# Kernel optimization log

Measured on AMD Instinct MI355X. Metric: run time of the kernel, lower is better.

## Reference

```python
import jax, jax.numpy as jnp
import numpy as np

EPS = 1e-08


def setup_inputs() -> dict:
    key = jax.random.key(0)
    k1, k2 = jax.random.split(key)
    query_features = jax.random.normal(k1, (64, 1024, 32, 32), dtype=jnp.float32)
    support_features = jax.random.normal(k2, (25, 1024, 32, 32), dtype=jnp.float32)
    return {"query_features": query_features, "support_features": support_features}


def reference(query_features, support_features):
    B, C, h, w = support_features.shape
    NQ = query_features.shape[0]
    # Covariance over channels: flatten support to (C, B*h*w), center, GEMM.
    support = jnp.transpose(support_features, (1, 0, 2, 3)).reshape(C, -1)
    centered = support - jnp.mean(support, axis=1, keepdims=True)
    N = B * h * w
    cov = (centered @ centered.T) / (N - 1 + EPS)  # (C, C)
    # Queries: (NQ, C, d), L2-normalize each channel row over spatial dim.
    q = query_features.reshape(NQ, C, -1)
    q = q / (jnp.linalg.norm(q, axis=2, keepdims=True) + EPS)
    # diag(q^T cov q) without materializing (d, d): cov@q then elementwise reduce over C.
    cq = jnp.einsum('cD,nDd->ncd', cov, q)  # (NQ, C, d)
    scores = jnp.mean(jnp.sum(q * cq, axis=1), axis=1)  # (NQ,)
    return scores
```

## Files before the change

### kernel.cpp

```cpp
#include <hip/hip_runtime.h>

#define NQ   64
#define CCH  1024
#define DSP  1024
#define NSUP 25600
#define NK_COV 50

typedef __attribute__((ext_vector_type(4))) float f32x4;
typedef __attribute__((ext_vector_type(8))) __bf16 bf16x8;

#define WAITVM(N) asm volatile("s_waitcnt vmcnt(" #N ")" ::: "memory")
#define WAITLGKM0() asm volatile("s_waitcnt lgkmcnt(0)" ::: "memory")
#define BAR() __builtin_amdgcn_s_barrier()
#define SCHED0() __builtin_amdgcn_sched_barrier(0)

__device__ inline unsigned short f2bf(float x) {
  unsigned u = __builtin_bit_cast(unsigned, x);
  u += 0x7fffu + ((u >> 16) & 1u);
  return (unsigned short)(u >> 16);
}

__global__ __launch_bounds__(256) void zero_kernel(float4* __restrict__ cov4,
                                                   float4* __restrict__ out4) {
  const int i = blockIdx.x * 256 + threadIdx.x;
  cov4[i] = make_float4(0.f, 0.f, 0.f, 0.f);
  if (i < 16) out4[i] = make_float4(0.f, 0.f, 0.f, 0.f);
}


__global__ __launch_bounds__(512) void mean_center_kernel(
    const float* __restrict__ sup, float* __restrict__ mean,
    unsigned short* __restrict__ Sb, int write_sb) {
  __shared__ float4 row[6400];
  __shared__ float red[512];
  const int c = blockIdx.x;
  const int tid = threadIdx.x;
  float s = 0.f;
  for (int qd = tid; qd < 6400; qd += 512) {
    const int b = qd >> 8, s4 = (qd & 255) << 2;
    const float4 v = *(const float4*)(sup + ((size_t)b * CCH + c) * DSP + s4);
    row[qd] = v;
    s += v.x + v.y + v.z + v.w;
  }
  red[tid] = s;
  __syncthreads();
  for (int st = 256; st > 0; st >>= 1) {
    if (tid < st) red[tid] += red[tid + st];
    __syncthreads();
  }
  const float m = red[0] * (1.0f / 25600.0f);
  if (tid == 0) mean[c] = m;
  if (write_sb) {
    for (int qd = tid; qd < 6400; qd += 512) {
      const float4 v = row[qd];
      const int b = qd >> 8, s4 = (qd & 255) << 2;
      ushort4 o;
      o.x = f2bf(v.x - m); o.y = f2bf(v.y - m);
      o.z = f2bf(v.z - m); o.w = f2bf(v.w - m);
      *(ushort4*)(Sb + (size_t)c * NSUP + b * DSP + s4) = o;
    }
  }
}

__global__ __launch_bounds__(256) void qnorm_kernel(
    const float* __restrict__ q, float* __restrict__ qfac,
    unsigned short* __restrict__ Qb, int write_qb) {
  const int row = blockIdx.x * 4 + (threadIdx.x >> 6);
  const int l = threadIdx.x & 63;
  const float4* src = (const float4*)(q + (size_t)row * DSP);
  float4 v[4];
  float ss = 0.f;
#pragma unroll
  for (int i = 0; i < 4; ++i) {
    v[i] = src[l + 64 * i];
    ss += v[i].x * v[i].x + v[i].y * v[i].y + v[i].z * v[i].z + v[i].w * v[i].w;
  }
#pragma unroll
  for (int off = 32; off > 0; off >>= 1) ss += __shfl_xor(ss, off);
  const float f = 1.0f / (sqrtf(ss) + 1e-8f);
  if (l == 0) qfac[row] = f;
  if (write_qb) {
#pragma unroll
    for (int i = 0; i < 4; ++i) {
      ushort4 o;
      o.x = f2bf(v[i].x * f); o.y = f2bf(v[i].y * f);
      o.z = f2bf(v[i].z * f); o.w = f2bf(v[i].w * f);
      *(ushort4*)(Qb + (size_t)row * DSP + (size_t)(l + 64 * i) * 4) = o;
    }
  }
}


__device__ inline void rd4(const unsigned short* base, int r0, int col, int lr, bf16x8 f[4]) {
#pragma unroll
  for (int i = 0; i < 4; ++i)
    f[i] = *(const bf16x8*)(const void*)(base + (r0 + i * 16 + lr) * 64 + col);
}
__device__ inline void mfma16(const bf16x8 a[4], const bf16x8 b[4], f32x4 (*acc)[4]) {
  __builtin_amdgcn_s_setprio(1);
#pragma unroll
  for (int i = 0; i < 4; ++i)
#pragma unroll
    for (int j = 0; j < 4; ++j)
      acc[i][j] = __builtin_amdgcn_mfma_f32_16x16x32_bf16(a[i], b[j], acc[i][j], 0, 0, 0);
  __builtin_amdgcn_s_setprio(0);
}

__device__ inline void stage_glds(const unsigned short* __restrict__ src, int ld,
                                  int row0, int k0, unsigned short* lds) {
  const int tid = threadIdx.x;
  const int w = tid >> 6;
#pragma unroll
  for (int it = 0; it < 4; ++it) {
    const int ci = it * 256 + tid;
    const int r = ci >> 3;
    const int kc = ((ci & 7) ^ (r & 7)) << 3;
    const unsigned short* g = src + (size_t)(row0 + r) * ld + k0 + kc;
    unsigned short* lb = lds + ((it * 256 + w * 64) << 3);
    __builtin_amdgcn_global_load_lds((const __attribute__((address_space(1))) void*)g,
                                     (__attribute__((address_space(3))) void*)lb,
                                     16, 0, 0);
  }
}

__device__ inline void stage256g(const unsigned short* __restrict__ src, int ld,
                                 int row0, int k0, unsigned short* lds_base) {
  const int tid = threadIdx.x;
  const int wid = tid >> 6;
#pragma unroll
  for (int it = 0; it < 4; ++it) {
    const int ci = it * 512 + tid;
    const int r = ci >> 3;
    const int kc = ((ci & 7) ^ (r & 7)) << 3;
    const unsigned short* g = src + (size_t)(row0 + r) * ld + k0 + kc;
    unsigned short* lb = lds_base + ((it * 512 + (wid << 6)) << 3);
    __builtin_amdgcn_global_load_lds((const __attribute__((address_space(1))) void*)g,
                                     (__attribute__((address_space(3))) void*)lb,
                                     16, 0, 0);
  }
}

template <int NT>
__device__ inline void loop256(const unsigned short* __restrict__ src, int ld,
                               int rowA, int rowB, int k0, bool diag,
                               unsigned short* lds,
                               int wm, int wn, int lr, int kg, int sw,
                               f32x4 (*acc)[4]) {
  stage256g(src, ld, rowA, k0, lds);
  if (!diag) stage256g(src, ld, rowB, k0, lds + 16384);
  stage256g(src, ld, rowA, k0 + 64, lds + 32768);
  if (!diag) stage256g(src, ld, rowB, k0 + 64, lds + 32768 + 16384);

  for (int t = 0; t < NT; ++t) {
    const int cb = (t & 1) << 15;
    if (t < NT - 1) { if (diag) { WAITVM(4); } else { WAITVM(8); } }
    else { WAITVM(0); }
    BAR(); SCHED0();
    const unsigned short* A = lds + cb + wm * 8192;
    const unsigned short* B = lds + cb + (diag ? 0 : 16384) + (wn >> 1) * 8192;
    const int brow = (wn & 1) * 64;
    bf16x8 a[4], b[4];
    {
      const int col = kg ^ sw;
      rd4(B, brow, col, lr, b);
      rd4(A, 0, col, lr, a);
      mfma16(a, b, &acc[0]);
      rd4(A, 64, col, lr, a);
      mfma16(a, b, &acc[4]);
    }
    {
      const int col = (32 + kg) ^ sw;
      rd4(B, brow, col, lr, b);
      rd4(A, 0, col, lr, a);
      mfma16(a, b, &acc[0]);
      rd4(A, 64, col, lr, a);
      WAITLGKM0();
      BAR(); SCHED0();
      if (t + 2 < NT) {
        stage256g(src, ld, rowA, k0 + (t + 2) * 64, lds + cb);
        if (!diag) stage256g(src, ld, rowB, k0 + (t + 2) * 64, lds + cb + 16384);
      }
      mfma16(a, b, &acc[4]);
    }
  }
}

__device__ inline void decode_tile8(int t, int& ti, int& tj) {
  int rem = t; ti = 0;
  while (rem >= 8 - ti) { rem -= 8 - ti; ++ti; }
  tj = ti + rem;
}
__device__ inline void decode_pair4(int p, int& ti, int& tj) {
  int rem = p; ti = 0;
  while (rem >= 4 - ti) { rem -= 4 - ti; ++ti; }
  tj = ti + rem;
}

__global__ __launch_bounds__(256) void cov128_kernel(
    const unsigned short* __restrict__ Sb, float* __restrict__ cov) {
  __shared__ unsigned short clds[32768];
  const int wg = blockIdx.x;
  const int ks = wg & 7;
  int ti, tj; decode_tile8(wg >> 3, ti, tj);
  const bool diag = (ti == tj);
  const bool mirror = (!(ti & 1)) && (tj == ti + 1);
  const int tid = threadIdx.x, l = tid & 63, w = tid >> 6;
  const int wr = (w >> 1) * 64, wc = (w & 1) * 64, lr = l & 15, kg = (l >> 4) * 8;
  const int sw = (lr & 7) << 3;
  f32x4 acc[4][4];
#pragma unroll
  for (int i = 0; i < 4; ++i)
#pragma unroll
    for (int j = 0; j < 4; ++j) acc[i][j] = 0.f;

  const int kbase = ks * (NSUP / 8);

  stage_glds(Sb, NSUP, ti * 128, kbase, clds);
  if (!diag) stage_glds(Sb, NSUP, tj * 128, kbase, clds + 8192);
  stage_glds(Sb, NSUP, ti * 128, kbase + 64, clds + 16384);
  if (!diag) stage_glds(Sb, NSUP, tj * 128, kbase + 64, clds + 16384 + 8192);
  for (int t = 0; t < NK_COV; ++t) {
    const int cb = (t & 1) * 16384;
    if (t < NK_COV - 1) { if (diag) { WAITVM(4); } else { WAITVM(8); } }
    else { WAITVM(0); }
    BAR(); SCHED0();
    const unsigned short* A = clds + cb;
    const unsigned short* B = diag ? A : A + 8192;
    bf16x8 a[4], b[4];
    {
      const int col = kg ^ sw;
      rd4(A, wr, col, lr, a);
      rd4(B, wc, col, lr, b);
      mfma16(a, b, (f32x4(*)[4])acc);
    }
    {
      const int col = (32 + kg) ^ sw;
      rd4(A, wr, col, lr, a);
      rd4(B, wc, col, lr, b);
      WAITLGKM0();
      BAR(); SCHED0();
      if (t + 2 < NK_COV) {
        const int k2 = kbase + (t + 2) * 64;
        stage_glds(Sb, NSUP, ti * 128, k2, clds + cb);
        if (!diag) stage_glds(Sb, NSUP, tj * 128, k2, clds + cb + 8192);
      }
      mfma16(a, b, (f32x4(*)[4])acc);
    }
  }

  const float scale = 1.0f / (25599.0f + 1e-8f);
  const int rbase = ti * 128 + wr + (l >> 4) * 4;
  const int cbase = tj * 128 + wc + (l & 15);
#pragma unroll
  for (int i = 0; i < 4; ++i)
#pragma unroll
    for (int j = 0; j < 4; ++j)
#pragma unroll
      for (int r = 0; r < 4; ++r) {
        const float v = acc[i][j][r] * scale;
        atomicAdd(&cov[(size_t)(rbase + i * 16 + r) * CCH + cbase + j * 16], v);
        if (mirror)
          atomicAdd(&cov[(size_t)(cbase + j * 16) * CCH + rbase + i * 16 + r], v);
      }
}

__global__ __launch_bounds__(512, 2) void gram256_kernel(
    const unsigned short* __restrict__ Qb, const float* __restrict__ cov,
    float* __restrict__ out) {
  __shared__ unsigned short lds[65536];
  const int wg = blockIdx.x;
  const int xcd = wg & 7, slot = wg >> 3;
  const int n = xcd * 8 + slot / 10;
  int ti, tj; decode_pair4(slot % 10, ti, tj);
  const bool diag = (ti == tj);
  const int tid = threadIdx.x, l = tid & 63, wid = tid >> 6;
  const int wm = wid >> 2, wn = wid & 3;
  const int lr = l & 15, kg = (l >> 4) * 8;
  const int sw = (lr & 7) << 3;
  const unsigned short* Qn = Qb + (size_t)n * CCH * DSP;

  f32x4 acc[8][4];
#pragma unroll
  for (int i = 0; i < 8; ++i)
#pragma unroll
    for (int j = 0; j < 4; ++j) acc[i][j] = 0.f;

  loop256<16>(Qn, DSP, ti * 256, tj * 256, 0, diag, lds,
              wm, wn, lr, kg, sw, acc);

  float s = 0.f;
  const int rbase = ti * 256 + wm * 128 + (l >> 4) * 4;
  const int cbase = tj * 256 + wn * 64 + (l & 15);
#pragma unroll
  for (int i = 0; i < 8; ++i)
#pragma unroll
    for (int j = 0; j < 4; ++j)
#pragma unroll
      for (int r = 0; r < 4; ++r)
        s += acc[i][j][r] * cov[(size_t)(rbase + i * 16 + r) * CCH + cbase + j * 16];
  if (!diag) s *= 2.0f;
  s *= (1.0f / 1024.0f);
#pragma unroll
  for (int off = 32; off > 0; off >>= 1) s += __shfl_xor(s, off);
  if (l == 0) atomicAdd(&out[n], s);
}

__device__ inline void mfma16s(const bf16x8 a[4], const bf16x8 b[4], f32x4 acc[4][4]) {
#pragma unroll
  for (int i = 0; i < 4; ++i)
#pragma unroll
    for (int j = 0; j < 4; ++j)
      acc[i][j] = __builtin_amdgcn_mfma_f32_16x16x32_bf16(a[i], b[j], acc[i][j], 0, 0, 0);
}

__device__ inline void stage_sup_f32(const float* __restrict__ sup,
                                     const float* __restrict__ mean,
                                     int row0, int k0, unsigned short* lds) {
  const int tid = threadIdx.x;
#pragma unroll
  for (int it = 0; it < 4; ++it) {
    const int ci = it * 256 + tid;
    const int r = ci >> 3, kc = (ci & 7) << 3;
    const int c = row0 + r;
    const int k = k0 + kc;
    const int b = k >> 10, sp = k & 1023;
    const float4* gp = (const float4*)(sup + ((size_t)b * CCH + c) * DSP + sp);
    const float4 v0 = gp[0], v1 = gp[1];
    const float m = mean[c];
    union { unsigned short h[8]; int4 q; } pk;
    pk.h[0] = f2bf(v0.x - m); pk.h[1] = f2bf(v0.y - m);
    pk.h[2] = f2bf(v0.z - m); pk.h[3] = f2bf(v0.w - m);
    pk.h[4] = f2bf(v1.x - m); pk.h[5] = f2bf(v1.y - m);
    pk.h[6] = f2bf(v1.z - m); pk.h[7] = f2bf(v1.w - m);
    *(int4*)(lds + (size_t)(r * 8 + ((ci & 7) ^ (r & 7))) * 8) = pk.q;
  }
}
__device__ inline void stage_q_f32(const float* __restrict__ qn,
                                   const float* __restrict__ qfacn,
                                   int row0, int k0, unsigned short* lds) {
  const int tid = threadIdx.x;
#pragma unroll
  for (int it = 0; it < 4; ++it) {
    const int ci = it * 256 + tid;
    const int r = ci >> 3, kc = (ci & 7) << 3;
    const int c = row0 + r;
    const float4* gp = (const float4*)(qn + (size_t)c * DSP + k0 + kc);
    const float4 v0 = gp[0], v1 = gp[1];
    const float f = qfacn[c];
    union { unsigned short h[8]; int4 q; } pk;
    pk.h[0] = f2bf(v0.x * f); pk.h[1] = f2bf(v0.y * f);
    pk.h[2] = f2bf(v0.z * f); pk.h[3] = f2bf(v0.w * f);
    pk.h[4] = f2bf(v1.x * f); pk.h[5] = f2bf(v1.y * f);
    pk.h[6] = f2bf(v1.z * f); pk.h[7] = f2bf(v1.w * f);
    *(int4*)(lds + (size_t)(r * 8 + ((ci & 7) ^ (r & 7))) * 8) = pk.q;
  }
}
__device__ inline void compute_step(const unsigned short* lA, const unsigned short* lB,
                                    int wr, int wc, int lr, int kg, f32x4 acc[4][4]) {
  const int sc = (lr & 7) << 3;
#pragma unroll
  for (int kk = 0; kk < 64; kk += 32) {
    const int col = (kk + kg) ^ sc;
    bf16x8 a[4], b[4];
    rd4(lA, wr, col, lr, a);
    rd4(lB, wc, col, lr, b);
    mfma16s(a, b, acc);
  }
}

__global__ __launch_bounds__(256) void cov_kernel_f32(
    const float* __restrict__ sup, const float* __restrict__ mean,
    float* __restrict__ cov) {
  __shared__ unsigned short clds[32768];
  const int wg = blockIdx.x;
  const int ks = wg & 7;
  int ti, tj; decode_tile8(wg >> 3, ti, tj);
  const bool diag = (ti == tj);
  const int tid = threadIdx.x, l = tid & 63, w = tid >> 6;
  const int wr = (w >> 1) * 64, wc = (w & 1) * 64, lr = l & 15, kg = (l >> 4) * 8;
  f32x4 acc[4][4];
#pragma unroll
  for (int i = 0; i < 4; ++i)
#pragma unroll
    for (int j = 0; j < 4; ++j) acc[i][j] = 0.f;

  const int kbase = ks * (NSUP / 8);
  stage_sup_f32(sup, mean, ti * 128, kbase, clds);
  if (!diag) stage_sup_f32(sup, mean, tj * 128, kbase, clds + 8192);
  __syncthreads();
  for (int kt = 0; kt < 50; ++kt) {
    const int cb = (kt & 1) * 16384;
    const int nb = cb ^ 16384;
    if (kt + 1 < 50) {
      const int k1 = kbase + (kt + 1) * 64;
      stage_sup_f32(sup, mean, ti * 128, k1, clds + nb);
      if (!diag) stage_sup_f32(sup, mean, tj * 128, k1, clds + nb + 8192);
    }
    compute_step(clds + cb, diag ? clds + cb : clds + cb + 8192, wr, wc, lr, kg, acc);
    __syncthreads();
  }
  const float scale = 1.0f / (25599.0f + 1e-8f);
  const int rbase = ti * 128 + wr + (l >> 4) * 4;
  const int cbase = tj * 128 + wc + (l & 15);
#pragma unroll
  for (int i = 0; i < 4; ++i)
#pragma unroll
    for (int j = 0; j < 4; ++j)
#pragma unroll
      for (int r = 0; r < 4; ++r)
        atomicAdd(&cov[(size_t)(rbase + i * 16 + r) * CCH + cbase + j * 16],
                  acc[i][j][r] * scale);
}

__global__ __launch_bounds__(256) void gram_kernel_f32(
    const float* __restrict__ q, const float* __restrict__ qfac,
    const float* __restrict__ cov, float* __restrict__ out) {
  __shared__ unsigned short lA[2][128 * 64];
  __shared__ unsigned short lB[2][128 * 64];
  const int wg = blockIdx.x;
  const int xcd = wg & 7, slot = wg >> 3;
  const int n = xcd * 8 + slot / 36;
  int ti, tj; decode_tile8(slot % 36, ti, tj);
  const bool diag = (ti == tj);
  const int tid = threadIdx.x, l = tid & 63, w = tid >> 6;
  const int wr = (w >> 1) * 64, wc = (w & 1) * 64, lr = l & 15, kg = (l >> 4) * 8;
  f32x4 acc[4][4];
#pragma unroll
  for (int i = 0; i < 4; ++i)
#pragma unroll
    for (int j = 0; j < 4; ++j) acc[i][j] = 0.f;

  const float* qn = q + (size_t)n * CCH * DSP;
  const float* qfacn = qfac + (size_t)n * CCH;

  stage_q_f32(qn, qfacn, ti * 128, 0, lA[0]);
  if (!diag) stage_q_f32(qn, qfacn, tj * 128, 0, lB[0]);
  __syncthreads();
  int cur = 0;
  for (int kt = 0; kt < 16; ++kt) {
    if (kt + 1 < 16) {
      const int k1 = (kt + 1) * 64;
      stage_q_f32(qn, qfacn, ti * 128, k1, lA[cur ^ 1]);
      if (!diag) stage_q_f32(qn, qfacn, tj * 128, k1, lB[cur ^ 1]);
    }
    compute_step(lA[cur], diag ? lA[cur] : lB[cur], wr, wc, lr, kg, acc);
    __syncthreads();
    cur ^= 1;
  }

  float s = 0.f;
  const int rbase = ti * 128 + wr + (l >> 4) * 4;
  const int cbase = tj * 128 + wc + (l & 15);
#pragma unroll
  for (int i = 0; i < 4; ++i)
#pragma unroll
    for (int j = 0; j < 4; ++j)
#pragma unroll
      for (int r = 0; r < 4; ++r)
        s += acc[i][j][r] * cov[(size_t)(rbase + i * 16 + r) * CCH + cbase + j * 16];
  if (!diag) s *= 2.0f;
  s *= (1.0f / 1024.0f);
#pragma unroll
  for (int off = 32; off > 0; off >>= 1) s += __shfl_xor(s, off);
  if (l == 0) atomicAdd(&out[n], s);
}

extern "C" void kernel_launch(void* const* d_in, const int* in_sizes, int n_in,
                              void* d_out, int out_size, void* d_ws, size_t ws_size,
                              hipStream_t stream) {
  const float* q = (const float*)d_in[0];
  const float* sup = (const float*)d_in[1];
  float* out = (float*)d_out;

  char* ws = (char*)d_ws;
  float* mean = (float*)ws;
  float* qfac = (float*)(ws + (4 << 10));
  float* cov  = (float*)(ws + (4 << 10) + (256 << 10));
  unsigned short* Sb = (unsigned short*)(ws + (4 << 10) + (256 << 10) + (4 << 20));
  unsigned short* Qb = Sb + (size_t)CCH * NSUP;
  const size_t need_fat = (size_t)(4 << 10) + (256 << 10) + (4 << 20) +
                          (size_t)CCH * NSUP * 2 + (size_t)NQ * CCH * DSP * 2;
  const bool fat = ws_size >= need_fat;

  zero_kernel<<<1024, 256, 0, stream>>>((float4*)cov, (float4*)out);

  mean_center_kernel<<<CCH, 512, 0, stream>>>(sup, mean, Sb, fat ? 1 : 0);
  qnorm_kernel<<<NQ * CCH / 4, 256, 0, stream>>>(q, qfac, Qb, fat ? 1 : 0);

  if (fat) {
    cov128_kernel<<<dim3(288), 256, 0, stream>>>(Sb, cov);
    gram256_kernel<<<dim3(640), 512, 0, stream>>>(Qb, cov, out);
  } else {
    cov_kernel_f32<<<dim3(288), 256, 0, stream>>>(sup, mean, cov);
    gram_kernel_f32<<<dim3(8 * 8 * 36), 256, 0, stream>>>(q, qfac, cov, out);
  }
}
```

Before: 279.3 us.

## Interleave LDS reads with MFMA via barriers and exploit symmetry in gram epilogue

The LDS-read/MFMA sequence in both GEMM main loops is restructured with extra workgroup barriers and lgkmcnt waits between each read-and-compute phase, so waves issue MFMA in lockstep. The cov kernel stops writing mirrored atomic adds for the adjacent off-diagonal tiles. The gram epilogue on diagonal tiles instead weights the upper 128x128 off-diagonal quadrant by 2 and skips the lower one, relying on symmetry of the Gram block and of cov. Extra barriers add synchronisation cost. Correctness depends on the cov matrix being symmetric where the gram epilogue now reads it, which the removed mirror writes previously supplied.

```diff
diff --git a/kernel.cpp b/kernel.cpp
--- a/kernel.cpp
+++ b/kernel.cpp
@@ -159,29 +159,30 @@
     const unsigned short* A = lds + cb + wm * 8192;
     const unsigned short* B = lds + cb + (diag ? 0 : 16384) + (wn >> 1) * 8192;
     const int brow = (wn & 1) * 64;
+    const int col0 = kg ^ sw, col1 = (32 + kg) ^ sw;
     bf16x8 a[4], b[4];
-    {
-      const int col = kg ^ sw;
-      rd4(B, brow, col, lr, b);
-      rd4(A, 0, col, lr, a);
-      mfma16(a, b, &acc[0]);
-      rd4(A, 64, col, lr, a);
-      mfma16(a, b, &acc[4]);
-    }
-    {
-      const int col = (32 + kg) ^ sw;
-      rd4(B, brow, col, lr, b);
-      rd4(A, 0, col, lr, a);
-      mfma16(a, b, &acc[0]);
-      rd4(A, 64, col, lr, a);
-      WAITLGKM0();
-      BAR(); SCHED0();
-      if (t + 2 < NT) {
-        stage256g(src, ld, rowA, k0 + (t + 2) * 64, lds + cb);
-        if (!diag) stage256g(src, ld, rowB, k0 + (t + 2) * 64, lds + cb + 16384);
-      }
-      mfma16(a, b, &acc[4]);
-    }
+    rd4(B, brow, col0, lr, b);
+    rd4(A, 0, col0, lr, a);
+    BAR(); WAITLGKM0(); SCHED0();
+    mfma16(a, b, &acc[0]);
+    BAR();
+    rd4(A, 64, col0, lr, a);
+    BAR(); WAITLGKM0(); SCHED0();
+    mfma16(a, b, &acc[4]);
+    BAR();
+    rd4(B, brow, col1, lr, b);
+    rd4(A, 0, col1, lr, a);
+    BAR(); WAITLGKM0(); SCHED0();
+    mfma16(a, b, &acc[0]);
+    BAR();
+    rd4(A, 64, col1, lr, a);
+    WAITLGKM0();
+    BAR(); SCHED0();
+    if (t + 2 < NT) {
+      stage256g(src, ld, rowA, k0 + (t + 2) * 64, lds + cb);
+      if (!diag) stage256g(src, ld, rowB, k0 + (t + 2) * 64, lds + cb + 16384);
+    }
+    mfma16(a, b, &acc[4]);
   }
 }
 
@@ -203,7 +204,6 @@
   const int ks = wg & 7;
   int ti, tj; decode_tile8(wg >> 3, ti, tj);
   const bool diag = (ti == tj);
-  const bool mirror = (!(ti & 1)) && (tj == ti + 1);
   const int tid = threadIdx.x, l = tid & 63, w = tid >> 6;
   const int wr = (w >> 1) * 64, wc = (w & 1) * 64, lr = l & 15, kg = (l >> 4) * 8;
   const int sw = (lr & 7) << 3;
@@ -226,26 +226,23 @@
     BAR(); SCHED0();
     const unsigned short* A = clds + cb;
     const unsigned short* B = diag ? A : A + 8192;
+    const int col0 = kg ^ sw, col1 = (32 + kg) ^ sw;
     bf16x8 a[4], b[4];
-    {
-      const int col = kg ^ sw;
-      rd4(A, wr, col, lr, a);
-      rd4(B, wc, col, lr, b);
-      mfma16(a, b, (f32x4(*)[4])acc);
-    }
-    {
-      const int col = (32 + kg) ^ sw;
-      rd4(A, wr, col, lr, a);
-      rd4(B, wc, col, lr, b);
-      WAITLGKM0();
-      BAR(); SCHED0();
-      if (t + 2 < NK_COV) {
-        const int k2 = kbase + (t + 2) * 64;
-        stage_glds(Sb, NSUP, ti * 128, k2, clds + cb);
-        if (!diag) stage_glds(Sb, NSUP, tj * 128, k2, clds + cb + 8192);
-      }
-      mfma16(a, b, (f32x4(*)[4])acc);
-    }
+    rd4(A, wr, col0, lr, a);
+    rd4(B, wc, col0, lr, b);
+    BAR(); WAITLGKM0(); SCHED0();
+    mfma16(a, b, (f32x4(*)[4])acc);
+    BAR();
+    rd4(A, wr, col1, lr, a);
+    rd4(B, wc, col1, lr, b);
+    WAITLGKM0();
+    BAR(); SCHED0();
+    if (t + 2 < NK_COV) {
+      const int k2 = kbase + (t + 2) * 64;
+      stage_glds(Sb, NSUP, ti * 128, k2, clds + cb);
+      if (!diag) stage_glds(Sb, NSUP, tj * 128, k2, clds + cb + 8192);
+    }
+    mfma16(a, b, (f32x4(*)[4])acc);
   }
 
   const float scale = 1.0f / (25599.0f + 1e-8f);
@@ -256,12 +253,9 @@
 #pragma unroll
     for (int j = 0; j < 4; ++j)
 #pragma unroll
-      for (int r = 0; r < 4; ++r) {
-        const float v = acc[i][j][r] * scale;
-        atomicAdd(&cov[(size_t)(rbase + i * 16 + r) * CCH + cbase + j * 16], v);
-        if (mirror)
-          atomicAdd(&cov[(size_t)(cbase + j * 16) * CCH + rbase + i * 16 + r], v);
-      }
+      for (int r = 0; r < 4; ++r)
+        atomicAdd(&cov[(size_t)(rbase + i * 16 + r) * CCH + cbase + j * 16],
+                  acc[i][j][r] * scale);
 }
 
 __global__ __launch_bounds__(512, 2) void gram256_kernel(
@@ -288,18 +282,25 @@
   loop256<16>(Qn, DSP, ti * 256, tj * 256, 0, diag, lds,
               wm, wn, lr, kg, sw, acc);
 
+  float wgt;
+  if (!diag) wgt = 2.0f;
+  else if (wm == 0 && (wn >> 1) == 1) wgt = 2.0f;
+  else if (wm == 1 && (wn >> 1) == 0) wgt = 0.0f;
+  else wgt = 1.0f;
+
   float s = 0.f;
-  const int rbase = ti * 256 + wm * 128 + (l >> 4) * 4;
-  const int cbase = tj * 256 + wn * 64 + (l & 15);
-#pragma unroll
-  for (int i = 0; i < 8; ++i)
-#pragma unroll
-    for (int j = 0; j < 4; ++j)
-#pragma unroll
-      for (int r = 0; r < 4; ++r)
-        s += acc[i][j][r] * cov[(size_t)(rbase + i * 16 + r) * CCH + cbase + j * 16];
-  if (!diag) s *= 2.0f;
-  s *= (1.0f / 1024.0f);
+  if (wgt != 0.0f) {
+    const int rbase = ti * 256 + wm * 128 + (l >> 4) * 4;
+    const int cbase = tj * 256 + wn * 64 + (l & 15);
+#pragma unroll
+    for (int i = 0; i < 8; ++i)
+#pragma unroll
+      for (int j = 0; j < 4; ++j)
+#pragma unroll
+        for (int r = 0; r < 4; ++r)
+          s += acc[i][j][r] * cov[(size_t)(rbase + i * 16 + r) * CCH + cbase + j * 16];
+  }
+  s *= wgt * (1.0f / 1024.0f);
 #pragma unroll
   for (int off = 32; off > 0; off >>= 1) s += __shfl_xor(s, off);
   if (l == 0) atomicAdd(&out[n], s);
```

After: 275.4 us. About the same (-1.4%).
